# Kernel tuning notes

Hardware: AMD Instinct MI355X
Metric: run time of the kernel (lower is better)

The kernel has to match this reference:

```python
import jax, jax.numpy as jnp
import numpy as np

B, S, D = 2, 2048, 2048
H, KVH, HD = 8, 1, 256
N_REP = H // KVH
WIN = 1024
THETA = 10000.0
SCALE = 1.0 / (HD ** 0.5)


def setup_inputs() -> dict:
    key = jax.random.key(0)
    k1, k2, k3, k4, k5 = jax.random.split(key, 5)
    hidden_states = jax.random.normal(k1, (B, S, D), dtype=jnp.float32)
    neg = jnp.finfo(jnp.float32).min
    causal = jnp.where(jnp.tril(jnp.ones((S, S), jnp.float32)) == 1.0, 0.0, neg)
    attention_mask = jnp.broadcast_to(causal[None, None], (B, 1, S, S)).copy()
    position_ids = jnp.broadcast_to(jnp.arange(S, dtype=jnp.int32)[None, :], (B, S)).copy()
    std = 0.02
    Wq = std * jax.random.normal(k2, (H * HD, D), dtype=jnp.float32)
    Wk = std * jax.random.normal(k3, (KVH * HD, D), dtype=jnp.float32)
    Wv = std * jax.random.normal(k4, (KVH * HD, D), dtype=jnp.float32)
    Wo = std * jax.random.normal(k5, (D, H * HD), dtype=jnp.float32)
    return {"hidden_states": hidden_states, "attention_mask": attention_mask,
            "position_ids": position_ids, "Wq": Wq, "Wk": Wk, "Wv": Wv, "Wo": Wo}


def _rotate_half(x):
    x1, x2 = x[..., : HD // 2], x[..., HD // 2:]
    return jnp.concatenate([-x2, x1], axis=-1)


def _rope(position_ids):
    inv_freq = 1.0 / (THETA ** (jnp.arange(0, HD, 2, dtype=jnp.float32) / HD))  # [HD/2]
    freqs = position_ids.astype(jnp.float32)[:, :, None] * inv_freq  # [b,s,HD/2]
    emb = jnp.concatenate([freqs, freqs], axis=-1)  # [b,s,HD]
    # unsqueeze at head dim -> [b,1,s,HD]
    return jnp.cos(emb)[:, None], jnp.sin(emb)[:, None]


def reference(hidden_states, attention_mask, position_ids, Wq, Wk, Wv, Wo):
    b, s, _ = hidden_states.shape
    q = (hidden_states @ Wq.T).reshape(b, s, H, HD).transpose(0, 2, 1, 3)    # [b,H,s,hd]
    k = (hidden_states @ Wk.T).reshape(b, s, KVH, HD).transpose(0, 2, 1, 3)  # [b,KVH,s,hd]
    v = (hidden_states @ Wv.T).reshape(b, s, KVH, HD).transpose(0, 2, 1, 3)

    cos, sin = _rope(position_ids)
    q = q * cos + _rotate_half(q) * sin
    k = k * cos + _rotate_half(k) * sin

    neg = jnp.finfo(attention_mask.dtype).min
    ones = jnp.ones_like(attention_mask)
    sliding = jnp.triu(ones, -(WIN - 1)) * jnp.tril(ones, WIN - 1)
    mask = jnp.where(sliding == 1.0, attention_mask, neg)  # [b,1,s,s]

    # GQA without materializing repeated KV: group query heads by kv head
    qg = q.reshape(b, KVH, N_REP, s, HD)
    scores = jnp.einsum('bgrqd,bgkd->bgrqk', qg, k) * SCALE
    scores = scores + mask[:, :, None]  # broadcast over rep dim
    probs = jax.nn.softmax(scores, axis=-1)
    out = jnp.einsum('bgrqk,bgkd->bgrqd', probs, v)  # [b,KVH,rep,s,hd]
    out = out.reshape(b, H, s, HD).transpose(0, 2, 1, 3).reshape(b, s, H * HD)
    return out @ Wo.T
```

## Files before the change

### kernel.cpp

```cpp
#include <hip/hip_runtime.h>
#include <stdint.h>

typedef __attribute__((ext_vector_type(8))) short bf16x8;
typedef __attribute__((ext_vector_type(4))) float f32x4;
typedef __attribute__((ext_vector_type(4))) unsigned short u16x4;

#define LOG2E 1.44269504088896340736f
#define SCALE 0.0625f

__device__ __forceinline__ unsigned short f32_bf16(float f) {
  unsigned int u = __float_as_uint(f);
  u += 0x7fffu + ((u >> 16) & 1u);
  return (unsigned short)(u >> 16);
}
__device__ __forceinline__ float bf16_f32(unsigned short h) {
  return __uint_as_float(((unsigned int)h) << 16);
}

__device__ __forceinline__ void gload16(const unsigned short* g, unsigned short* l) {
  __builtin_amdgcn_global_load_lds((const __attribute__((address_space(1))) void*)g,
                                   (__attribute__((address_space(3))) void*)l, 16, 0, 0);
}

__global__ void cast_kernel(const float* __restrict__ in, unsigned short* __restrict__ out, int n4) {
  int i = blockIdx.x * blockDim.x + threadIdx.x;
  if (i >= n4) return;
  const float4 v = ((const float4*)in)[i];
  u16x4 o;
  o[0] = f32_bf16(v.x); o[1] = f32_bf16(v.y); o[2] = f32_bf16(v.z); o[3] = f32_bf16(v.w);
  ((u16x4*)out)[i] = o;
}

template<int OUTF32>
__global__ __launch_bounds__(256) void gemm_nt(const unsigned short* __restrict__ A,
                                               const unsigned short* __restrict__ B,
                                               void* __restrict__ Cp,
                                               int M, int N, int K) {
  __shared__ unsigned short As[2][128 * 32];
  __shared__ unsigned short Bs[2][128 * 32];
  const int t = threadIdx.x;
  const int lane = t & 63;
  const int wave = t >> 6;
  const int wr = (wave >> 1) * 64;
  const int wc = (wave & 1) * 64;
  const int l15 = lane & 15, lg = lane >> 4;

  const int gx = gridDim.x, gy = gridDim.y;
  int orig = blockIdx.y * gx + blockIdx.x;
  int nwg = gx * gy;
  int wg = orig;
  if ((nwg & 7) == 0) wg = (orig & 7) * (nwg >> 3) + (orig >> 3);
  const int bx = wg / gy, by = wg % gy;
  const long m0 = (long)by * 128;
  const long n0 = (long)bx * 128;

  f32x4 acc[4][4];
#pragma unroll
  for (int m = 0; m < 4; ++m)
#pragma unroll
    for (int n = 0; n < 4; ++n) acc[m][n] = (f32x4){0.f, 0.f, 0.f, 0.f};

  const int srow = t >> 2;
  const int scol = (t & 3) * 8;
  const unsigned short* Ag = A + (m0 + srow) * (long)K + scol;
  const unsigned short* Bg = B + (n0 + srow) * (long)K + scol;

  auto stage = [&](int buf, int k0) {
    gload16(Ag + k0, &As[buf][t * 8]);
    gload16(Ag + (long)64 * K + k0, &As[buf][2048 + t * 8]);
    gload16(Bg + k0, &Bs[buf][t * 8]);
    gload16(Bg + (long)64 * K + k0, &Bs[buf][2048 + t * 8]);
  };

  stage(0, 0);
  __syncthreads();
  int cur = 0;
  for (int k0 = 0; k0 < K; k0 += 32) {
    if (k0 + 32 < K) stage(cur ^ 1, k0 + 32);
    bf16x8 af[4], bfr[4];
#pragma unroll
    for (int m = 0; m < 4; ++m) af[m] = *(const bf16x8*)&As[cur][(wr + m * 16 + l15) * 32 + lg * 8];
#pragma unroll
    for (int n = 0; n < 4; ++n) bfr[n] = *(const bf16x8*)&Bs[cur][(wc + n * 16 + l15) * 32 + lg * 8];
    __builtin_amdgcn_s_setprio(1);
#pragma unroll
    for (int m = 0; m < 4; ++m)
#pragma unroll
      for (int n = 0; n < 4; ++n)
        acc[m][n] = __builtin_amdgcn_mfma_f32_16x16x32_bf16(af[m], bfr[n], acc[m][n], 0, 0, 0);
    __builtin_amdgcn_s_setprio(0);
    __syncthreads();
    cur ^= 1;
  }

#pragma unroll
  for (int m = 0; m < 4; ++m)
#pragma unroll
    for (int n = 0; n < 4; ++n)
#pragma unroll
      for (int r = 0; r < 4; ++r) {
        long row = m0 + wr + m * 16 + lg * 4 + r;
        long col = n0 + wc + n * 16 + l15;
        if (OUTF32)
          ((float*)Cp)[row * N + col] = acc[m][n][r];
        else
          ((unsigned short*)Cp)[row * N + col] = f32_bf16(acc[m][n][r]);
      }
}

__global__ void rope_table(const int* __restrict__ pos, float* __restrict__ ctab,
                           float* __restrict__ stab) {
  int i = blockIdx.x * blockDim.x + threadIdx.x;
  int d = i & 127;
  int s = (i >> 7) & 2047;
  int b = i >> 18;
  float p = (float)pos[b * 2048 + s];
  float f = p * exp2f(-(float)d * 0.10381025296523f);
  float sn, c;
  sincosf(f, &sn, &c);
  ctab[i] = c;
  stab[i] = sn;
}

__global__ void rope_apply(unsigned short* __restrict__ qkv, const float* __restrict__ ctab,
                           const float* __restrict__ stab) {
  int i = blockIdx.x * blockDim.x + threadIdx.x;
  int g = i & 15;
  int hh = (i >> 4) % 9;
  int sb_ = (i >> 4) / 9;
  int s = sb_ & 2047;
  int b = sb_ >> 11;
  size_t base = (size_t)(b * 2048 + s) * 2560 + (hh == 8 ? 2048 : hh * 256) + g * 8;
  const float* ct = ctab + ((size_t)(b * 2048 + s) << 7) + g * 8;
  const float* st = stab + ((size_t)(b * 2048 + s) << 7) + g * 8;
  bf16x8 lo = *(const bf16x8*)(qkv + base);
  bf16x8 hi = *(const bf16x8*)(qkv + base + 128);
  bf16x8 lo2, hi2;
#pragma unroll
  for (int e = 0; e < 8; ++e) {
    float c = ct[e], sn = st[e];
    float x1 = bf16_f32((unsigned short)lo[e]);
    float x2 = bf16_f32((unsigned short)hi[e]);
    lo2[e] = (short)f32_bf16(x1 * c - x2 * sn);
    hi2[e] = (short)f32_bf16(x2 * c + x1 * sn);
  }
  *(bf16x8*)(qkv + base) = lo2;
  *(bf16x8*)(qkv + base + 128) = hi2;
}

__global__ __launch_bounds__(256) void transpose_v(const unsigned short* __restrict__ qkv,
                                                   unsigned short* __restrict__ vt) {
  __shared__ unsigned short tile[64][68];
  const int t = threadIdx.x;
  const int s0 = blockIdx.x * 64, d0 = blockIdx.y * 64, b = blockIdx.z;
  const int r = t >> 4, c4 = (t & 15) * 4;
#pragma unroll
  for (int j = 0; j < 4; ++j) {
    int row = r + j * 16;
    const unsigned short* src = qkv + (size_t)(b * 2048 + s0 + row) * 2560 + 2304 + d0 + c4;
#pragma unroll
    for (int e = 0; e < 4; ++e) tile[row][c4 + e] = src[e];
  }
  __syncthreads();
#pragma unroll
  for (int j = 0; j < 4; ++j) {
    int drow = r + j * 16;
    u16x4 o;
#pragma unroll
    for (int e = 0; e < 4; ++e) o[e] = tile[c4 + e][drow];
    *(u16x4*)(vt + (size_t)(b * 256 + d0 + drow) * 2048 + s0 + c4) = o;
  }
}

__global__ __launch_bounds__(256) void attn2(const unsigned short* __restrict__ qkv,
                                             const unsigned short* __restrict__ vt,
                                             unsigned short* __restrict__ O) {
  __shared__ __align__(16) unsigned short Ks[2][32 * 256];
  __shared__ __align__(16) unsigned short Vs[2][256 * 32];
  const int t = threadIdx.x, lane = t & 63, wave = t >> 6;
  const int l15 = lane & 15, lg = lane >> 4;
  const int qb = blockIdx.x, h = blockIdx.y, b = blockIdx.z;
  const int q0 = qb * 64;
  const int qg = q0 + wave * 16 + l15;

  bf16x8 qf[8];
  {
    const unsigned short* qp = qkv + (size_t)(b * 2048 + qg) * 2560 + h * 256 + lg * 8;
#pragma unroll
    for (int c = 0; c < 8; ++c) qf[c] = *(const bf16x8*)(qp + c * 32);
  }

  size_t kgb[4], vgb[4];
  int klo[4], vlo[4];
#pragma unroll
  for (int p = 0; p < 4; ++p) {
    int i = p * 256 + t;
    int kr = i >> 5, kb = (i & 31) << 4;
    int ksrc = kb ^ ((kr & 7) << 4);
    kgb[p] = (size_t)(b * 2048 + kr) * 2560 + 2048 + (ksrc >> 1);
    klo[p] = i * 8;
    int vr = i >> 2, vb = (i & 3) << 4;
    int vsrc = vb ^ (((vr >> 1) & 3) << 4);
    vgb[p] = (size_t)(b * 256 + vr) * 2048 + (vsrc >> 1);
    vlo[p] = i * 8;
  }

  f32x4 oacc[16];
#pragma unroll
  for (int dt = 0; dt < 16; ++dt) oacc[dt] = (f32x4){0.f, 0.f, 0.f, 0.f};
  float mrun = -3e30f, lrun = 0.f;

  int ks0 = q0 - 1023;
  if (ks0 < 0) ks0 = 0;
  ks0 &= ~31;
  const int nst = (q0 + 64 - ks0) >> 5;

#pragma unroll
  for (int p = 0; p < 4; ++p) gload16(qkv + kgb[p] + (size_t)ks0 * 2560, &Ks[0][klo[p]]);
#pragma unroll
  for (int p = 0; p < 4; ++p) gload16(vt + vgb[p] + ks0, &Vs[0][vlo[p]]);
  __syncthreads();

  for (int si = 0; si < nst; ++si) {
    const int ks = ks0 + si * 32;
    const int cur = si & 1;
    if (si + 1 < nst) {
      const size_t ko = (size_t)(ks + 32) * 2560;
#pragma unroll
      for (int p = 0; p < 4; ++p) gload16(qkv + kgb[p] + ko, &Ks[cur ^ 1][klo[p]]);
#pragma unroll
      for (int p = 0; p < 4; ++p) gload16(vt + vgb[p] + (ks + 32), &Vs[cur ^ 1][vlo[p]]);
    }
    const unsigned short* Kc = Ks[cur];
    const unsigned short* Vc = Vs[cur];

    f32x4 sa = (f32x4){0.f, 0.f, 0.f, 0.f};
    f32x4 sb2 = (f32x4){0.f, 0.f, 0.f, 0.f};
    const int kswz = (l15 & 7) << 4;
    __builtin_amdgcn_s_setprio(1);
#pragma unroll
    for (int c = 0; c < 8; ++c) {
      const int off = ((c * 64 + lg * 16) ^ kswz) >> 1;
      bf16x8 k0 = *(const bf16x8*)&Kc[l15 * 256 + off];
      bf16x8 k1 = *(const bf16x8*)&Kc[(16 + l15) * 256 + off];
      sa = __builtin_amdgcn_mfma_f32_16x16x32_bf16(k0, qf[c], sa, 0, 0, 0);
      sb2 = __builtin_amdgcn_mfma_f32_16x16x32_bf16(k1, qf[c], sb2, 0, 0, 0);
    }
    __builtin_amdgcn_s_setprio(0);

    float pv[8];
    const int kb0 = ks + lg * 4, kb1 = kb0 + 16;
    const int lo_b = qg - 1024;
#pragma unroll
    for (int r = 0; r < 4; ++r) {
      int k0i = kb0 + r, k1i = kb1 + r;
      pv[r] = (k0i <= qg && k0i > lo_b) ? sa[r] * SCALE : -3e38f;
      pv[4 + r] = (k1i <= qg && k1i > lo_b) ? sb2[r] * SCALE : -3e38f;
    }
    float mx = fmaxf(fmaxf(fmaxf(pv[0], pv[1]), fmaxf(pv[2], pv[3])),
                     fmaxf(fmaxf(pv[4], pv[5]), fmaxf(pv[6], pv[7])));
    mx = fmaxf(mx, __shfl_xor(mx, 16));
    mx = fmaxf(mx, __shfl_xor(mx, 32));
    if (!__all(mx - mrun <= 8.0f)) {
      float mnew = fmaxf(mrun, mx);
      float al = exp2f((mrun - mnew) * LOG2E);
#pragma unroll
      for (int dt = 0; dt < 16; ++dt) oacc[dt] *= al;
      lrun *= al;
      mrun = mnew;
    }
    float ps = 0.f;
#pragma unroll
    for (int j = 0; j < 8; ++j) {
      pv[j] = exp2f((pv[j] - mrun) * LOG2E);
      ps += pv[j];
    }
    ps += __shfl_xor(ps, 16);
    ps += __shfl_xor(ps, 32);
    lrun += ps;

    unsigned int w0 = ((unsigned int)f32_bf16(pv[1]) << 16) | f32_bf16(pv[0]);
    unsigned int w1 = ((unsigned int)f32_bf16(pv[3]) << 16) | f32_bf16(pv[2]);
    unsigned int w2 = ((unsigned int)f32_bf16(pv[5]) << 16) | f32_bf16(pv[4]);
    unsigned int w3 = ((unsigned int)f32_bf16(pv[7]) << 16) | f32_bf16(pv[6]);
    unsigned int sA0 = (lg < 2) ? w2 : w0;
    unsigned int sA1 = (lg < 2) ? w3 : w1;
    unsigned int rA0 = (unsigned int)__shfl_xor((int)sA0, 32);
    unsigned int rA1 = (unsigned int)__shfl_xor((int)sA1, 32);
    unsigned int own0 = (lg < 2) ? w0 : w2;
    unsigned int own1 = (lg < 2) ? w1 : w3;
    const bool sendOwn = ((lg ^ (lg >> 1)) & 1) != 0;
    unsigned int sB0 = sendOwn ? own0 : rA0;
    unsigned int sB1 = sendOwn ? own1 : rA1;
    unsigned int rB0 = (unsigned int)__shfl_xor((int)sB0, 16);
    unsigned int rB1 = (unsigned int)__shfl_xor((int)sB1, 16);
    union { unsigned int u[4]; bf16x8 v; } pu;
    pu.u[0] = (lg == 0) ? own0 : ((lg == 2) ? rA0 : rB0);
    pu.u[1] = (lg == 0) ? own1 : ((lg == 2) ? rA1 : rB1);
    pu.u[2] = (lg == 3) ? own0 : ((lg == 1) ? rA0 : rB0);
    pu.u[3] = (lg == 3) ? own1 : ((lg == 1) ? rA1 : rB1);

    const int vswz = (lg * 16) ^ (((l15 >> 1) & 3) << 4);
    __builtin_amdgcn_s_setprio(1);
#pragma unroll
    for (int dt = 0; dt < 16; ++dt) {
      bf16x8 vf = *(const bf16x8*)&Vc[(dt * 16 + l15) * 32 + (vswz >> 1)];
      oacc[dt] = __builtin_amdgcn_mfma_f32_16x16x32_bf16(vf, pu.v, oacc[dt], 0, 0, 0);
    }
    __builtin_amdgcn_s_setprio(0);
    __syncthreads();
  }

  float inv = 1.0f / lrun;
  unsigned short* op = O + (size_t)(b * 2048 + qg) * 2048 + h * 256 + lg * 4;
#pragma unroll
  for (int dt = 0; dt < 16; ++dt) {
    u16x4 o4;
#pragma unroll
    for (int r = 0; r < 4; ++r) o4[r] = f32_bf16(oacc[dt][r] * inv);
    *(u16x4*)(op + dt * 16) = o4;
  }
}

extern "C" void kernel_launch(void* const* d_in, const int* in_sizes, int n_in,
                              void* d_out, int out_size, void* d_ws, size_t ws_size,
                              hipStream_t stream) {
  const float* hidden = (const float*)d_in[0];
  const int* pos_ids = (const int*)d_in[2];
  const float* Wq = (const float*)d_in[3];
  const float* Wk = (const float*)d_in[4];
  const float* Wv = (const float*)d_in[5];
  const float* Wo = (const float*)d_in[6];
  float* out = (float*)d_out;
  char* ws = (char*)d_ws;

  unsigned short* qkv_bf = (unsigned short*)(ws);
  unsigned short* hid_bf = (unsigned short*)(ws + 20971520);
  unsigned short* w_bf   = (unsigned short*)(ws + 37748736);
  unsigned short* vtbuf  = (unsigned short*)(ws + 48234496);
  float*          ctab   = (float*)(ws + 50331648);
  float*          stab   = (float*)(ws + 52428800);
  unsigned short* attno  = hid_bf;

  cast_kernel<<<8192, 256, 0, stream>>>(hidden, hid_bf, 2097152);
  cast_kernel<<<4096, 256, 0, stream>>>(Wq, w_bf, 1048576);
  cast_kernel<<<512, 256, 0, stream>>>(Wk, w_bf + 4194304, 131072);
  cast_kernel<<<512, 256, 0, stream>>>(Wv, w_bf + 4718592, 131072);

  gemm_nt<0><<<dim3(20, 32), 256, 0, stream>>>(hid_bf, w_bf, qkv_bf, 4096, 2560, 2048);

  cast_kernel<<<4096, 256, 0, stream>>>(Wo, w_bf, 1048576);

  rope_table<<<2048, 256, 0, stream>>>(pos_ids, ctab, stab);
  rope_apply<<<2304, 256, 0, stream>>>(qkv_bf, ctab, stab);

  transpose_v<<<dim3(32, 4, 2), 256, 0, stream>>>(qkv_bf, vtbuf);

  attn2<<<dim3(32, 8, 2), 256, 0, stream>>>(qkv_bf, vtbuf, attno);

  gemm_nt<1><<<dim3(16, 32), 256, 0, stream>>>(attno, w_bf, out, 4096, 2048, 2048);
}
```

Baseline: 338.9 us.

## Replace 128x128 GEMM with 256x256 tile, 8-wave, triple-buffered pipelined kernel

Both projection GEMMs now use 256x256 output tiles computed by 512 threads (8 waves of 128x64), which raises data reuse per loaded byte. A three-stage LDS ring with direct global-to-LDS loads and explicit vmcnt/lgkmcnt waits and barriers interleaves prefetch with two half-tile MFMA phases. The grids shrink to 160 and 128 workgroups, which is fewer than the CU count of the chip and risks underutilization. The larger accumulator array also raises register pressure.

```diff
diff --git a/kernel.cpp b/kernel.cpp
--- a/kernel.cpp
+++ b/kernel.cpp
@@ -32,17 +32,17 @@
 }
 
 template<int OUTF32>
-__global__ __launch_bounds__(256) void gemm_nt(const unsigned short* __restrict__ A,
-                                               const unsigned short* __restrict__ B,
-                                               void* __restrict__ Cp,
-                                               int M, int N, int K) {
-  __shared__ unsigned short As[2][128 * 32];
-  __shared__ unsigned short Bs[2][128 * 32];
+__global__ __launch_bounds__(512, 2) void gemm256(const unsigned short* __restrict__ A,
+                                                  const unsigned short* __restrict__ B,
+                                                  void* __restrict__ Cp,
+                                                  int M, int N, int K) {
+  __shared__ unsigned short As[3 * 8192];
+  __shared__ unsigned short Bs[3 * 8192];
   const int t = threadIdx.x;
   const int lane = t & 63;
   const int wave = t >> 6;
-  const int wr = (wave >> 1) * 64;
-  const int wc = (wave & 1) * 64;
+  const int wr = (wave >> 2) * 128;
+  const int wc = (wave & 3) * 64;
   const int l15 = lane & 15, lg = lane >> 4;
 
   const int gx = gridDim.x, gy = gridDim.y;
@@ -51,37 +51,52 @@
   int wg = orig;
   if ((nwg & 7) == 0) wg = (orig & 7) * (nwg >> 3) + (orig >> 3);
   const int bx = wg / gy, by = wg % gy;
-  const long m0 = (long)by * 128;
-  const long n0 = (long)bx * 128;
-
-  f32x4 acc[4][4];
-#pragma unroll
-  for (int m = 0; m < 4; ++m)
+  const long m0 = (long)by * 256;
+  const long n0 = (long)bx * 256;
+
+  f32x4 acc[8][4];
+#pragma unroll
+  for (int m = 0; m < 8; ++m)
 #pragma unroll
     for (int n = 0; n < 4; ++n) acc[m][n] = (f32x4){0.f, 0.f, 0.f, 0.f};
 
   const int srow = t >> 2;
   const int scol = (t & 3) * 8;
-  const unsigned short* Ag = A + (m0 + srow) * (long)K + scol;
-  const unsigned short* Bg = B + (n0 + srow) * (long)K + scol;
-
-  auto stage = [&](int buf, int k0) {
-    gload16(Ag + k0, &As[buf][t * 8]);
-    gload16(Ag + (long)64 * K + k0, &As[buf][2048 + t * 8]);
-    gload16(Bg + k0, &Bs[buf][t * 8]);
-    gload16(Bg + (long)64 * K + k0, &Bs[buf][2048 + t * 8]);
-  };
-
-  stage(0, 0);
-  __syncthreads();
-  int cur = 0;
-  for (int k0 = 0; k0 < K; k0 += 32) {
-    if (k0 + 32 < K) stage(cur ^ 1, k0 + 32);
-    bf16x8 af[4], bfr[4];
-#pragma unroll
-    for (int m = 0; m < 4; ++m) af[m] = *(const bf16x8*)&As[cur][(wr + m * 16 + l15) * 32 + lg * 8];
-#pragma unroll
-    for (int n = 0; n < 4; ++n) bfr[n] = *(const bf16x8*)&Bs[cur][(wc + n * 16 + l15) * 32 + lg * 8];
+  const unsigned short* Ag0 = A + (m0 + srow) * (size_t)K + scol;
+  const unsigned short* Ag1 = Ag0 + (size_t)128 * K;
+  const unsigned short* Bg0 = B + (n0 + srow) * (size_t)K + scol;
+  const unsigned short* Bg1 = Bg0 + (size_t)128 * K;
+  const int NT = K >> 5;
+
+  gload16(Ag0, &As[t * 8]);
+  gload16(Ag1, &As[4096 + t * 8]);
+  gload16(Bg0, &Bs[t * 8]);
+  gload16(Bg1, &Bs[4096 + t * 8]);
+  gload16(Ag0 + 32, &As[8192 + t * 8]);
+  gload16(Ag1 + 32, &As[8192 + 4096 + t * 8]);
+  gload16(Bg0 + 32, &Bs[8192 + t * 8]);
+  gload16(Bg1 + 32, &Bs[8192 + 4096 + t * 8]);
+  asm volatile("s_waitcnt vmcnt(4)" ::: "memory");
+  __builtin_amdgcn_s_barrier();
+
+  int bc = 0, bsg = 2;
+  for (int kt = 0; kt < NT; ++kt) {
+    const unsigned short* Ac = &As[bc * 8192];
+    const unsigned short* Bc = &Bs[bc * 8192];
+    const bool st = (kt + 2) < NT;
+    const int c2 = (kt + 2) << 5;
+
+    bf16x8 bfr[4], af[4];
+#pragma unroll
+    for (int n = 0; n < 4; ++n) bfr[n] = *(const bf16x8*)(Bc + (wc + n * 16 + l15) * 32 + lg * 8);
+#pragma unroll
+    for (int m = 0; m < 4; ++m) af[m] = *(const bf16x8*)(Ac + (wr + m * 16 + l15) * 32 + lg * 8);
+    if (st) {
+      gload16(Ag0 + c2, &As[bsg * 8192 + t * 8]);
+      gload16(Ag1 + c2, &As[bsg * 8192 + 4096 + t * 8]);
+    }
+    __builtin_amdgcn_s_barrier();
+    asm volatile("s_waitcnt lgkmcnt(0)" ::: "memory");
     __builtin_amdgcn_s_setprio(1);
 #pragma unroll
     for (int m = 0; m < 4; ++m)
@@ -89,12 +104,34 @@
       for (int n = 0; n < 4; ++n)
         acc[m][n] = __builtin_amdgcn_mfma_f32_16x16x32_bf16(af[m], bfr[n], acc[m][n], 0, 0, 0);
     __builtin_amdgcn_s_setprio(0);
-    __syncthreads();
-    cur ^= 1;
-  }
-
-#pragma unroll
-  for (int m = 0; m < 4; ++m)
+    __builtin_amdgcn_s_barrier();
+
+#pragma unroll
+    for (int m = 0; m < 4; ++m) af[m] = *(const bf16x8*)(Ac + (wr + 64 + m * 16 + l15) * 32 + lg * 8);
+    if (st) {
+      gload16(Bg0 + c2, &Bs[bsg * 8192 + t * 8]);
+      gload16(Bg1 + c2, &Bs[bsg * 8192 + 4096 + t * 8]);
+      asm volatile("s_waitcnt vmcnt(4)" ::: "memory");
+    } else if (kt + 1 < NT) {
+      asm volatile("s_waitcnt vmcnt(0)" ::: "memory");
+    }
+    __builtin_amdgcn_s_barrier();
+    asm volatile("s_waitcnt lgkmcnt(0)" ::: "memory");
+    __builtin_amdgcn_s_setprio(1);
+#pragma unroll
+    for (int m = 0; m < 4; ++m)
+#pragma unroll
+      for (int n = 0; n < 4; ++n)
+        acc[4 + m][n] = __builtin_amdgcn_mfma_f32_16x16x32_bf16(af[m], bfr[n], acc[4 + m][n], 0, 0, 0);
+    __builtin_amdgcn_s_setprio(0);
+    __builtin_amdgcn_s_barrier();
+
+    bc = (bc == 2) ? 0 : bc + 1;
+    bsg = (bsg == 2) ? 0 : bsg + 1;
+  }
+
+#pragma unroll
+  for (int m = 0; m < 8; ++m)
 #pragma unroll
     for (int n = 0; n < 4; ++n)
 #pragma unroll
@@ -347,7 +384,7 @@
   cast_kernel<<<512, 256, 0, stream>>>(Wk, w_bf + 4194304, 131072);
   cast_kernel<<<512, 256, 0, stream>>>(Wv, w_bf + 4718592, 131072);
 
-  gemm_nt<0><<<dim3(20, 32), 256, 0, stream>>>(hid_bf, w_bf, qkv_bf, 4096, 2560, 2048);
+  gemm256<0><<<dim3(10, 16), 512, 0, stream>>>(hid_bf, w_bf, qkv_bf, 4096, 2560, 2048);
 
   cast_kernel<<<4096, 256, 0, stream>>>(Wo, w_bf, 1048576);
 
@@ -358,5 +395,5 @@
 
   attn2<<<dim3(32, 8, 2), 256, 0, stream>>>(qkv_bf, vtbuf, attno);
 
-  gemm_nt<1><<<dim3(16, 32), 256, 0, stream>>>(attno, w_bf, out, 4096, 2048, 2048);
-}
+  gemm256<1><<<dim3(8, 16), 512, 0, stream>>>(attno, w_bf, out, 4096, 2048, 2048);
+}
```

After: 366.1 us. +8.0%, slower.

## Fuse prep kernels, fold softmax scale into Q, stream V from global, skip dead tiles

Applied to the files above, without the earlier changes.

The four casts and the RoPE table build are merged into one `prep` launch. RoPE apply, the V transpose and the Wo cast are merged into one `mid` launch, and the attention scale is folded into Q during RoPE. The attention kernel now reads V fragments straight from global memory into registers instead of double-buffering them in LDS. Each wave skips key tiles that fall entirely outside its causal/sliding band and skips masking on fully-valid tiles. This cuts launch count, LDS traffic and wasted MFMA work, at the cost of uncoalesced-ish global V loads whose latency is no longer hidden by prefetch, plus extra bf16 rounding of the pre-scaled Q.

```diff
diff --git a/kernel.cpp b/kernel.cpp
--- a/kernel.cpp
+++ b/kernel.cpp
@@ -22,13 +22,42 @@
                                    (__attribute__((address_space(3))) void*)l, 16, 0, 0);
 }
 
-__global__ void cast_kernel(const float* __restrict__ in, unsigned short* __restrict__ out, int n4) {
-  int i = blockIdx.x * blockDim.x + threadIdx.x;
-  if (i >= n4) return;
+__device__ __forceinline__ void cast4(const float* __restrict__ in,
+                                      unsigned short* __restrict__ out, int i) {
   const float4 v = ((const float4*)in)[i];
   u16x4 o;
   o[0] = f32_bf16(v.x); o[1] = f32_bf16(v.y); o[2] = f32_bf16(v.z); o[3] = f32_bf16(v.w);
   ((u16x4*)out)[i] = o;
+}
+
+__global__ __launch_bounds__(256) void prep(const float* __restrict__ hidden,
+                                            const float* __restrict__ Wq,
+                                            const float* __restrict__ Wk,
+                                            const float* __restrict__ Wv,
+                                            const int* __restrict__ pos,
+                                            unsigned short* __restrict__ hid_bf,
+                                            unsigned short* __restrict__ w_bf,
+                                            float* __restrict__ ctab,
+                                            float* __restrict__ stab) {
+  int i = blockIdx.x * 256 + threadIdx.x;
+  if (i < 2097152) {
+    cast4(hidden, hid_bf, i);
+  } else if (i < 3145728) {
+    cast4(Wq, w_bf, i - 2097152);
+  } else if (i < 3276800) {
+    cast4(Wk, w_bf + 4194304, i - 3145728);
+  } else if (i < 3407872) {
+    cast4(Wv, w_bf + 4718592, i - 3276800);
+  } else {
+    int j = i - 3407872;
+    int d = j & 127, s = (j >> 7) & 2047, b = j >> 18;
+    float p = (float)pos[b * 2048 + s];
+    float f = p * exp2f(-(float)d * 0.10381025296523f);
+    float sn, c;
+    sincosf(f, &sn, &c);
+    ctab[j] = c;
+    stab[j] = sn;
+  }
 }
 
 template<int OUTF32>
@@ -108,80 +137,73 @@
       }
 }
 
-__global__ void rope_table(const int* __restrict__ pos, float* __restrict__ ctab,
-                           float* __restrict__ stab) {
-  int i = blockIdx.x * blockDim.x + threadIdx.x;
-  int d = i & 127;
-  int s = (i >> 7) & 2047;
-  int b = i >> 18;
-  float p = (float)pos[b * 2048 + s];
-  float f = p * exp2f(-(float)d * 0.10381025296523f);
-  float sn, c;
-  sincosf(f, &sn, &c);
-  ctab[i] = c;
-  stab[i] = sn;
-}
-
-__global__ void rope_apply(unsigned short* __restrict__ qkv, const float* __restrict__ ctab,
-                           const float* __restrict__ stab) {
-  int i = blockIdx.x * blockDim.x + threadIdx.x;
-  int g = i & 15;
-  int hh = (i >> 4) % 9;
-  int sb_ = (i >> 4) / 9;
-  int s = sb_ & 2047;
-  int b = sb_ >> 11;
-  size_t base = (size_t)(b * 2048 + s) * 2560 + (hh == 8 ? 2048 : hh * 256) + g * 8;
-  const float* ct = ctab + ((size_t)(b * 2048 + s) << 7) + g * 8;
-  const float* st = stab + ((size_t)(b * 2048 + s) << 7) + g * 8;
-  bf16x8 lo = *(const bf16x8*)(qkv + base);
-  bf16x8 hi = *(const bf16x8*)(qkv + base + 128);
-  bf16x8 lo2, hi2;
-#pragma unroll
-  for (int e = 0; e < 8; ++e) {
-    float c = ct[e], sn = st[e];
-    float x1 = bf16_f32((unsigned short)lo[e]);
-    float x2 = bf16_f32((unsigned short)hi[e]);
-    lo2[e] = (short)f32_bf16(x1 * c - x2 * sn);
-    hi2[e] = (short)f32_bf16(x2 * c + x1 * sn);
-  }
-  *(bf16x8*)(qkv + base) = lo2;
-  *(bf16x8*)(qkv + base + 128) = hi2;
-}
-
-__global__ __launch_bounds__(256) void transpose_v(const unsigned short* __restrict__ qkv,
-                                                   unsigned short* __restrict__ vt) {
+__global__ __launch_bounds__(256) void mid(unsigned short* __restrict__ qkv,
+                                           const float* __restrict__ ctab,
+                                           const float* __restrict__ stab,
+                                           unsigned short* __restrict__ vt,
+                                           const float* __restrict__ Wo,
+                                           unsigned short* __restrict__ wo_bf) {
   __shared__ unsigned short tile[64][68];
-  const int t = threadIdx.x;
-  const int s0 = blockIdx.x * 64, d0 = blockIdx.y * 64, b = blockIdx.z;
-  const int r = t >> 4, c4 = (t & 15) * 4;
-#pragma unroll
-  for (int j = 0; j < 4; ++j) {
-    int row = r + j * 16;
-    const unsigned short* src = qkv + (size_t)(b * 2048 + s0 + row) * 2560 + 2304 + d0 + c4;
-#pragma unroll
-    for (int e = 0; e < 4; ++e) tile[row][c4 + e] = src[e];
-  }
-  __syncthreads();
-#pragma unroll
-  for (int j = 0; j < 4; ++j) {
-    int drow = r + j * 16;
-    u16x4 o;
-#pragma unroll
-    for (int e = 0; e < 4; ++e) o[e] = tile[c4 + e][drow];
-    *(u16x4*)(vt + (size_t)(b * 256 + d0 + drow) * 2048 + s0 + c4) = o;
-  }
-}
-
-__global__ __launch_bounds__(256) void attn2(const unsigned short* __restrict__ qkv,
-                                             const unsigned short* __restrict__ vt,
-                                             unsigned short* __restrict__ O) {
+  const int bi = blockIdx.x, t = threadIdx.x;
+  if (bi < 2304) {
+    int i = bi * 256 + t;
+    int g = i & 15;
+    int hh = (i >> 4) % 9;
+    int sb_ = (i >> 4) / 9;
+    int s = sb_ & 2047, b = sb_ >> 11;
+    size_t base = (size_t)(b * 2048 + s) * 2560 + (hh == 8 ? 2048 : hh * 256) + g * 8;
+    const float* ct = ctab + ((size_t)(b * 2048 + s) << 7) + g * 8;
+    const float* st = stab + ((size_t)(b * 2048 + s) << 7) + g * 8;
+    const float sc = (hh == 8) ? 1.0f : SCALE;
+    bf16x8 lo = *(const bf16x8*)(qkv + base);
+    bf16x8 hi = *(const bf16x8*)(qkv + base + 128);
+    bf16x8 lo2, hi2;
+#pragma unroll
+    for (int e = 0; e < 8; ++e) {
+      float c = ct[e] * sc, sn = st[e] * sc;
+      float x1 = bf16_f32((unsigned short)lo[e]);
+      float x2 = bf16_f32((unsigned short)hi[e]);
+      lo2[e] = (short)f32_bf16(x1 * c - x2 * sn);
+      hi2[e] = (short)f32_bf16(x2 * c + x1 * sn);
+    }
+    *(bf16x8*)(qkv + base) = lo2;
+    *(bf16x8*)(qkv + base + 128) = hi2;
+  } else if (bi < 2560) {
+    int bb = bi - 2304;
+    const int s0 = (bb & 31) * 64, d0 = ((bb >> 5) & 3) * 64, b = bb >> 7;
+    const int r = t >> 4, c4 = (t & 15) * 4;
+#pragma unroll
+    for (int j = 0; j < 4; ++j) {
+      int row = r + j * 16;
+      const unsigned short* src = qkv + (size_t)(b * 2048 + s0 + row) * 2560 + 2304 + d0 + c4;
+#pragma unroll
+      for (int e = 0; e < 4; ++e) tile[row][c4 + e] = src[e];
+    }
+    __syncthreads();
+#pragma unroll
+    for (int j = 0; j < 4; ++j) {
+      int drow = r + j * 16;
+      u16x4 o;
+#pragma unroll
+      for (int e = 0; e < 4; ++e) o[e] = tile[c4 + e][drow];
+      *(u16x4*)(vt + (size_t)(b * 256 + d0 + drow) * 2048 + s0 + c4) = o;
+    }
+  } else {
+    int i = (bi - 2560) * 256 + t;
+    cast4(Wo, wo_bf, i);
+  }
+}
+
+__global__ __launch_bounds__(256, 2) void attn3(const unsigned short* __restrict__ qkv,
+                                                const unsigned short* __restrict__ vt,
+                                                unsigned short* __restrict__ O) {
   __shared__ __align__(16) unsigned short Ks[2][32 * 256];
-  __shared__ __align__(16) unsigned short Vs[2][256 * 32];
   const int t = threadIdx.x, lane = t & 63, wave = t >> 6;
   const int l15 = lane & 15, lg = lane >> 4;
   const int qb = blockIdx.x, h = blockIdx.y, b = blockIdx.z;
   const int q0 = qb * 64;
-  const int qg = q0 + wave * 16 + l15;
+  const int qw = q0 + wave * 16;
+  const int qg = qw + l15;
 
   bf16x8 qf[8];
   {
@@ -190,8 +212,8 @@
     for (int c = 0; c < 8; ++c) qf[c] = *(const bf16x8*)(qp + c * 32);
   }
 
-  size_t kgb[4], vgb[4];
-  int klo[4], vlo[4];
+  size_t kgb[4];
+  int klo[4];
 #pragma unroll
   for (int p = 0; p < 4; ++p) {
     int i = p * 256 + t;
@@ -199,11 +221,9 @@
     int ksrc = kb ^ ((kr & 7) << 4);
     kgb[p] = (size_t)(b * 2048 + kr) * 2560 + 2048 + (ksrc >> 1);
     klo[p] = i * 8;
-    int vr = i >> 2, vb = (i & 3) << 4;
-    int vsrc = vb ^ (((vr >> 1) & 3) << 4);
-    vgb[p] = (size_t)(b * 256 + vr) * 2048 + (vsrc >> 1);
-    vlo[p] = i * 8;
-  }
+  }
+
+  const unsigned short* vbase = vt + (size_t)b * 524288 + (size_t)l15 * 2048 + lg * 8;
 
   f32x4 oacc[16];
 #pragma unroll
@@ -217,8 +237,6 @@
 
 #pragma unroll
   for (int p = 0; p < 4; ++p) gload16(qkv + kgb[p] + (size_t)ks0 * 2560, &Ks[0][klo[p]]);
-#pragma unroll
-  for (int p = 0; p < 4; ++p) gload16(vt + vgb[p] + ks0, &Vs[0][vlo[p]]);
   __syncthreads();
 
   for (int si = 0; si < nst; ++si) {
@@ -228,86 +246,94 @@
       const size_t ko = (size_t)(ks + 32) * 2560;
 #pragma unroll
       for (int p = 0; p < 4; ++p) gload16(qkv + kgb[p] + ko, &Ks[cur ^ 1][klo[p]]);
-#pragma unroll
-      for (int p = 0; p < 4; ++p) gload16(vt + vgb[p] + (ks + 32), &Vs[cur ^ 1][vlo[p]]);
-    }
-    const unsigned short* Kc = Ks[cur];
-    const unsigned short* Vc = Vs[cur];
-
-    f32x4 sa = (f32x4){0.f, 0.f, 0.f, 0.f};
-    f32x4 sb2 = (f32x4){0.f, 0.f, 0.f, 0.f};
-    const int kswz = (l15 & 7) << 4;
-    __builtin_amdgcn_s_setprio(1);
-#pragma unroll
-    for (int c = 0; c < 8; ++c) {
-      const int off = ((c * 64 + lg * 16) ^ kswz) >> 1;
-      bf16x8 k0 = *(const bf16x8*)&Kc[l15 * 256 + off];
-      bf16x8 k1 = *(const bf16x8*)&Kc[(16 + l15) * 256 + off];
-      sa = __builtin_amdgcn_mfma_f32_16x16x32_bf16(k0, qf[c], sa, 0, 0, 0);
-      sb2 = __builtin_amdgcn_mfma_f32_16x16x32_bf16(k1, qf[c], sb2, 0, 0, 0);
-    }
-    __builtin_amdgcn_s_setprio(0);
-
-    float pv[8];
-    const int kb0 = ks + lg * 4, kb1 = kb0 + 16;
-    const int lo_b = qg - 1024;
-#pragma unroll
-    for (int r = 0; r < 4; ++r) {
-      int k0i = kb0 + r, k1i = kb1 + r;
-      pv[r] = (k0i <= qg && k0i > lo_b) ? sa[r] * SCALE : -3e38f;
-      pv[4 + r] = (k1i <= qg && k1i > lo_b) ? sb2[r] * SCALE : -3e38f;
-    }
-    float mx = fmaxf(fmaxf(fmaxf(pv[0], pv[1]), fmaxf(pv[2], pv[3])),
-                     fmaxf(fmaxf(pv[4], pv[5]), fmaxf(pv[6], pv[7])));
-    mx = fmaxf(mx, __shfl_xor(mx, 16));
-    mx = fmaxf(mx, __shfl_xor(mx, 32));
-    if (!__all(mx - mrun <= 8.0f)) {
-      float mnew = fmaxf(mrun, mx);
-      float al = exp2f((mrun - mnew) * LOG2E);
-#pragma unroll
-      for (int dt = 0; dt < 16; ++dt) oacc[dt] *= al;
-      lrun *= al;
-      mrun = mnew;
-    }
-    float ps = 0.f;
-#pragma unroll
-    for (int j = 0; j < 8; ++j) {
-      pv[j] = exp2f((pv[j] - mrun) * LOG2E);
-      ps += pv[j];
-    }
-    ps += __shfl_xor(ps, 16);
-    ps += __shfl_xor(ps, 32);
-    lrun += ps;
-
-    unsigned int w0 = ((unsigned int)f32_bf16(pv[1]) << 16) | f32_bf16(pv[0]);
-    unsigned int w1 = ((unsigned int)f32_bf16(pv[3]) << 16) | f32_bf16(pv[2]);
-    unsigned int w2 = ((unsigned int)f32_bf16(pv[5]) << 16) | f32_bf16(pv[4]);
-    unsigned int w3 = ((unsigned int)f32_bf16(pv[7]) << 16) | f32_bf16(pv[6]);
-    unsigned int sA0 = (lg < 2) ? w2 : w0;
-    unsigned int sA1 = (lg < 2) ? w3 : w1;
-    unsigned int rA0 = (unsigned int)__shfl_xor((int)sA0, 32);
-    unsigned int rA1 = (unsigned int)__shfl_xor((int)sA1, 32);
-    unsigned int own0 = (lg < 2) ? w0 : w2;
-    unsigned int own1 = (lg < 2) ? w1 : w3;
-    const bool sendOwn = ((lg ^ (lg >> 1)) & 1) != 0;
-    unsigned int sB0 = sendOwn ? own0 : rA0;
-    unsigned int sB1 = sendOwn ? own1 : rA1;
-    unsigned int rB0 = (unsigned int)__shfl_xor((int)sB0, 16);
-    unsigned int rB1 = (unsigned int)__shfl_xor((int)sB1, 16);
-    union { unsigned int u[4]; bf16x8 v; } pu;
-    pu.u[0] = (lg == 0) ? own0 : ((lg == 2) ? rA0 : rB0);
-    pu.u[1] = (lg == 0) ? own1 : ((lg == 2) ? rA1 : rB1);
-    pu.u[2] = (lg == 3) ? own0 : ((lg == 1) ? rA0 : rB0);
-    pu.u[3] = (lg == 3) ? own1 : ((lg == 1) ? rA1 : rB1);
-
-    const int vswz = (lg * 16) ^ (((l15 >> 1) & 3) << 4);
-    __builtin_amdgcn_s_setprio(1);
-#pragma unroll
-    for (int dt = 0; dt < 16; ++dt) {
-      bf16x8 vf = *(const bf16x8*)&Vc[(dt * 16 + l15) * 32 + (vswz >> 1)];
-      oacc[dt] = __builtin_amdgcn_mfma_f32_16x16x32_bf16(vf, pu.v, oacc[dt], 0, 0, 0);
-    }
-    __builtin_amdgcn_s_setprio(0);
+    }
+
+    const bool live = !((ks > qw + 15) || (ks + 31 <= qw - 1024));
+    if (live) {
+      bf16x8 vf[16];
+#pragma unroll
+      for (int dt = 0; dt < 16; ++dt)
+        vf[dt] = *(const bf16x8*)(vbase + (size_t)dt * 32768 + ks);
+
+      const unsigned short* Kc = Ks[cur];
+      f32x4 sa = (f32x4){0.f, 0.f, 0.f, 0.f};
+      f32x4 sb2 = (f32x4){0.f, 0.f, 0.f, 0.f};
+      const int kswz = (l15 & 7) << 4;
+      __builtin_amdgcn_s_setprio(1);
+#pragma unroll
+      for (int c = 0; c < 8; ++c) {
+        const int off = ((c * 64 + lg * 16) ^ kswz) >> 1;
+        bf16x8 k0 = *(const bf16x8*)&Kc[l15 * 256 + off];
+        bf16x8 k1 = *(const bf16x8*)&Kc[(16 + l15) * 256 + off];
+        sa = __builtin_amdgcn_mfma_f32_16x16x32_bf16(k0, qf[c], sa, 0, 0, 0);
+        sb2 = __builtin_amdgcn_mfma_f32_16x16x32_bf16(k1, qf[c], sb2, 0, 0, 0);
+      }
+      __builtin_amdgcn_s_setprio(0);
+
+      float pv[8];
+      const bool full = (ks + 31 <= qw) && (ks > qw - 1009);
+      if (full) {
+#pragma unroll
+        for (int r = 0; r < 4; ++r) { pv[r] = sa[r]; pv[4 + r] = sb2[r]; }
+      } else {
+        const int kb0 = ks + lg * 4, kb1 = kb0 + 16;
+        const int lo_b = qg - 1024;
+#pragma unroll
+        for (int r = 0; r < 4; ++r) {
+          int k0i = kb0 + r, k1i = kb1 + r;
+          pv[r] = (k0i <= qg && k0i > lo_b) ? sa[r] : -3e38f;
+          pv[4 + r] = (k1i <= qg && k1i > lo_b) ? sb2[r] : -3e38f;
+        }
+      }
+      float mx = fmaxf(fmaxf(fmaxf(pv[0], pv[1]), fmaxf(pv[2], pv[3])),
+                       fmaxf(fmaxf(pv[4], pv[5]), fmaxf(pv[6], pv[7])));
+      mx = fmaxf(mx, __shfl_xor(mx, 16));
+      mx = fmaxf(mx, __shfl_xor(mx, 32));
+      if (!__all(mx - mrun <= 8.0f)) {
+        float mnew = fmaxf(mrun, mx);
+        float al = exp2f((mrun - mnew) * LOG2E);
+#pragma unroll
+        for (int dt = 0; dt < 16; ++dt) oacc[dt] *= al;
+        lrun *= al;
+        mrun = mnew;
+      }
+      float ps = 0.f;
+#pragma unroll
+      for (int j = 0; j < 8; ++j) {
+        pv[j] = exp2f((pv[j] - mrun) * LOG2E);
+        ps += pv[j];
+      }
+      ps += __shfl_xor(ps, 16);
+      ps += __shfl_xor(ps, 32);
+      lrun += ps;
+
+      unsigned int w0 = ((unsigned int)f32_bf16(pv[1]) << 16) | f32_bf16(pv[0]);
+      unsigned int w1 = ((unsigned int)f32_bf16(pv[3]) << 16) | f32_bf16(pv[2]);
+      unsigned int w2 = ((unsigned int)f32_bf16(pv[5]) << 16) | f32_bf16(pv[4]);
+      unsigned int w3 = ((unsigned int)f32_bf16(pv[7]) << 16) | f32_bf16(pv[6]);
+      unsigned int sA0 = (lg < 2) ? w2 : w0;
+      unsigned int sA1 = (lg < 2) ? w3 : w1;
+      unsigned int rA0 = (unsigned int)__shfl_xor((int)sA0, 32);
+      unsigned int rA1 = (unsigned int)__shfl_xor((int)sA1, 32);
+      unsigned int own0 = (lg < 2) ? w0 : w2;
+      unsigned int own1 = (lg < 2) ? w1 : w3;
+      const bool sendOwn = ((lg ^ (lg >> 1)) & 1) != 0;
+      unsigned int sB0 = sendOwn ? own0 : rA0;
+      unsigned int sB1 = sendOwn ? own1 : rA1;
+      unsigned int rB0 = (unsigned int)__shfl_xor((int)sB0, 16);
+      unsigned int rB1 = (unsigned int)__shfl_xor((int)sB1, 16);
+      union { unsigned int u[4]; bf16x8 v; } pu;
+      pu.u[0] = (lg == 0) ? own0 : ((lg == 2) ? rA0 : rB0);
+      pu.u[1] = (lg == 0) ? own1 : ((lg == 2) ? rA1 : rB1);
+      pu.u[2] = (lg == 3) ? own0 : ((lg == 1) ? rA0 : rB0);
+      pu.u[3] = (lg == 3) ? own1 : ((lg == 1) ? rA1 : rB1);
+
+      __builtin_amdgcn_s_setprio(1);
+#pragma unroll
+      for (int dt = 0; dt < 16; ++dt)
+        oacc[dt] = __builtin_amdgcn_mfma_f32_16x16x32_bf16(vf[dt], pu.v, oacc[dt], 0, 0, 0);
+      __builtin_amdgcn_s_setprio(0);
+    }
     __syncthreads();
   }
 
@@ -342,21 +368,13 @@
   float*          stab   = (float*)(ws + 52428800);
   unsigned short* attno  = hid_bf;
 
-  cast_kernel<<<8192, 256, 0, stream>>>(hidden, hid_bf, 2097152);
-  cast_kernel<<<4096, 256, 0, stream>>>(Wq, w_bf, 1048576);
-  cast_kernel<<<512, 256, 0, stream>>>(Wk, w_bf + 4194304, 131072);
-  cast_kernel<<<512, 256, 0, stream>>>(Wv, w_bf + 4718592, 131072);
+  prep<<<15360, 256, 0, stream>>>(hidden, Wq, Wk, Wv, pos_ids, hid_bf, w_bf, ctab, stab);
 
   gemm_nt<0><<<dim3(20, 32), 256, 0, stream>>>(hid_bf, w_bf, qkv_bf, 4096, 2560, 2048);
 
-  cast_kernel<<<4096, 256, 0, stream>>>(Wo, w_bf, 1048576);
-
-  rope_table<<<2048, 256, 0, stream>>>(pos_ids, ctab, stab);
-  rope_apply<<<2304, 256, 0, stream>>>(qkv_bf, ctab, stab);
-
-  transpose_v<<<dim3(32, 4, 2), 256, 0, stream>>>(qkv_bf, vtbuf);
-
-  attn2<<<dim3(32, 8, 2), 256, 0, stream>>>(qkv_bf, vtbuf, attno);
+  mid<<<6656, 256, 0, stream>>>(qkv_bf, ctab, stab, vtbuf, Wo, w_bf);
+
+  attn3<<<dim3(32, 8, 2), 256, 0, stream>>>(qkv_bf, vtbuf, attno);
 
   gemm_nt<1><<<dim3(16, 32), 256, 0, stream>>>(attno, w_bf, out, 4096, 2048, 2048);
 }
```

Result: slower. 384.5 us (+13.5%).
